# Optimization experiments

Hardware: AMD Instinct MI355X
Metric: run time of the kernel (lower is better)

Reference implementation:

```python
import jax, jax.numpy as jnp
import numpy as np

B, S, D = 2, 2048, 1024
M = 2048          # d_mlp
E = 8             # num_experts
TOP_K = 2


def setup_inputs() -> dict:
    key = jax.random.key(0)
    ks = jax.random.split(key, 5)
    std = 0.02
    return {
        "residual": jax.random.normal(ks[0], (B, S, D), jnp.float32),
        "W_router": jax.random.normal(ks[1], (D, E), jnp.float32) * std,
        "W_gate": jax.random.normal(ks[2], (E, D, M), jnp.float32) * std,
        "b_gate": jnp.zeros((E, M), jnp.float32),
        "W_up": jax.random.normal(ks[3], (E, D, M), jnp.float32) * std,
        "b_up": jnp.zeros((E, M), jnp.float32),
        "W_out": jax.random.normal(ks[4], (E, M, D), jnp.float32) * std,
        "b_out": jnp.zeros((E, D), jnp.float32),
    }


def reference(residual, W_router, W_gate, b_gate, W_up, b_up, W_out, b_out):
    # --- router: softmax over experts, top-k selection, renormalize ---
    router_logits = jnp.einsum('bsd,de->bse', residual, W_router)
    router_probs = jax.nn.softmax(router_logits, axis=-1)
    top_k_probs, top_k_idx = jax.lax.top_k(router_probs, TOP_K)          # [B,S,K]
    top_k_probs = top_k_probs / (jnp.sum(top_k_probs, -1, keepdims=True) + 1e-8)
    # per-expert combine weight [B,S,E]; top-k indices are unique per token
    one_hot = jax.nn.one_hot(top_k_idx, E, dtype=residual.dtype)          # [B,S,K,E]
    expert_weights = jnp.einsum('bsk,bske->bse', top_k_probs, one_hot)
    # --- each expert runs dense SwiGLU MLP on the FULL batch (compute-then-mask, as in source) ---
    gate = jax.nn.silu(jnp.einsum('bsd,edm->ebsm', residual, W_gate) + b_gate[:, None, None, :])
    up = jnp.einsum('bsd,edm->ebsm', residual, W_up) + b_up[:, None, None, :]
    hidden = gate * up                                                    # [E,B,S,M]
    expert_out = jnp.einsum('ebsm,emd->ebsd', hidden, W_out) + b_out[:, None, None, :]
    # --- weighted combine (weights are zero for non-selected experts) ---
    output = jnp.einsum('bse,ebsd->bsd', expert_weights, expert_out)
    return output
```

## Files before the change

kernel.cpp:

```cpp
#include <hip/hip_runtime.h>
#include <cstdint>
#include <cstddef>

#define TT 4096
#define DD 1024
#define MM 2048
#define EE 8
#define NPAIR 8192

typedef unsigned short u16;
typedef __bf16 bf16x8 __attribute__((ext_vector_type(8)));
typedef float f32x4 __attribute__((ext_vector_type(4)));
typedef __attribute__((address_space(3))) void* lds_vp;
typedef __attribute__((address_space(1))) const void* gbl_cvp;

__device__ __forceinline__ void async16(u16* l, const u16* g) {
  __builtin_amdgcn_global_load_lds((gbl_cvp)(const void*)g, (lds_vp)(void*)l, 16, 0, 0);
}

__device__ __forceinline__ u16 f2bf(float f) {
  uint32_t u = __builtin_bit_cast(uint32_t, f);
  u += 0x7fffu + ((u >> 16) & 1u);
  return (u16)(u >> 16);
}
__device__ __forceinline__ float bf2f(u16 h) {
  uint32_t u = ((uint32_t)h) << 16;
  return __builtin_bit_cast(float, u);
}

__global__ void router_kernel(const float* __restrict__ X, const float* __restrict__ Wr,
                              int* __restrict__ tok_idx, float* __restrict__ wpair) {
  int wave = threadIdx.x >> 6;
  int lane = threadIdx.x & 63;
  int t = blockIdx.x * 4 + wave;
  const float4* x4 = (const float4*)(X + (size_t)t * DD);
  float acc[EE];
#pragma unroll
  for (int e = 0; e < EE; e++) acc[e] = 0.f;
#pragma unroll
  for (int i = 0; i < 4; i++) {
    float4 xv = x4[i * 64 + lane];
    const float4* wr4 = (const float4*)(Wr + (size_t)(i * 256 + lane * 4) * EE);
    float xs[4] = {xv.x, xv.y, xv.z, xv.w};
#pragma unroll
    for (int c = 0; c < 4; c++) {
      float4 wa = wr4[c * 2 + 0];
      float4 wb = wr4[c * 2 + 1];
      acc[0] += xs[c] * wa.x; acc[1] += xs[c] * wa.y;
      acc[2] += xs[c] * wa.z; acc[3] += xs[c] * wa.w;
      acc[4] += xs[c] * wb.x; acc[5] += xs[c] * wb.y;
      acc[6] += xs[c] * wb.z; acc[7] += xs[c] * wb.w;
    }
  }
#pragma unroll
  for (int off = 32; off > 0; off >>= 1)
#pragma unroll
    for (int e = 0; e < EE; e++) acc[e] += __shfl_xor(acc[e], off);
  if (lane == 0) {
    float mx = acc[0];
#pragma unroll
    for (int e = 1; e < EE; e++) mx = fmaxf(mx, acc[e]);
    float p[EE], s = 0.f;
#pragma unroll
    for (int e = 0; e < EE; e++) { p[e] = __expf(acc[e] - mx); s += p[e]; }
    float inv = 1.f / s;
#pragma unroll
    for (int e = 0; e < EE; e++) p[e] *= inv;
    int i0 = 0;
#pragma unroll
    for (int e = 1; e < EE; e++) if (p[e] > p[i0]) i0 = e;
    int i1 = (i0 == 0) ? 1 : 0;
#pragma unroll
    for (int e = 0; e < EE; e++) if (e != i0 && p[e] > p[i1]) i1 = e;
    float denom = p[i0] + p[i1] + 1e-8f;
    tok_idx[t * 2 + 0] = i0;
    tok_idx[t * 2 + 1] = i1;
    wpair[t * 2 + 0] = p[i0] / denom;
    wpair[t * 2 + 1] = p[i1] / denom;
  }
}

__global__ void bucket_kernel(const int* __restrict__ tok_idx, int* __restrict__ offsets,
                              int* __restrict__ bucket) {
  __shared__ int lcnt[EE];
  __shared__ int lcur[EE];
  int tid = threadIdx.x;
  if (tid < EE) lcnt[tid] = 0;
  __syncthreads();
  for (int i = tid; i < NPAIR; i += 1024) atomicAdd(&lcnt[tok_idx[i]], 1);
  __syncthreads();
  if (tid == 0) {
    int s = 0;
    for (int e = 0; e < EE; e++) {
      offsets[e] = s;
      lcur[e] = s;
      s += lcnt[e];
    }
    offsets[EE] = s;
  }
  __syncthreads();
  for (int i = tid; i < NPAIR; i += 1024) {
    int e = tok_idx[i];
    int pos = atomicAdd(&lcur[e], 1);
    bucket[pos] = i;
  }
}

__global__ void cvtx_kernel(const float* __restrict__ X, u16* __restrict__ Xbf) {
  int i = blockIdx.x * 256 + threadIdx.x;
  float4 v = ((const float4*)X)[i];
  ushort4 o;
  o.x = f2bf(v.x); o.y = f2bf(v.y); o.z = f2bf(v.z); o.w = f2bf(v.w);
  ((ushort4*)Xbf)[i] = o;
}

__global__ void transpose_cvt(const float* __restrict__ in, u16* __restrict__ out, int R, int C) {
  __shared__ float tile[32][33];
  int e = blockIdx.z;
  const float* I = in + (size_t)e * R * C;
  u16* O = out + (size_t)e * R * C;
  int c0 = blockIdx.x * 32, r0 = blockIdx.y * 32;
  for (int i = threadIdx.y; i < 32; i += 8)
    tile[i][threadIdx.x] = I[(size_t)(r0 + i) * C + c0 + threadIdx.x];
  __syncthreads();
  for (int i = threadIdx.y; i < 32; i += 8)
    O[(size_t)(c0 + i) * R + r0 + threadIdx.x] = f2bf(tile[threadIdx.x][i]);
}

template <int MODE>
__global__ __launch_bounds__(256)
void moe_gemm(const u16* __restrict__ Aglob, const u16* __restrict__ Wt,
              const float* __restrict__ bias, u16* __restrict__ Hws,
              float* __restrict__ Ypart, const int* __restrict__ offsets,
              const int* __restrict__ bucket, const float* __restrict__ wpair) {
  constexpr int K = (MODE == 2) ? MM : DD;
  constexpr int N = (MODE == 2) ? DD : MM;

  int x = blockIdx.x;
  int expert = -1, row0 = 0, rows = 0;
#pragma unroll 1
  for (int e = 0; e < EE; e++) {
    int o0 = offsets[e], o1 = offsets[e + 1];
    int nt = (o1 - o0 + 127) >> 7;
    if (x < nt) { expert = e; row0 = o0 + (x << 7); rows = min(128, o1 - row0); break; }
    x -= nt;
  }
  if (expert < 0) return;
  int n0 = blockIdx.y * 128;

  __shared__ u16 Alds[128 * 32];
  __shared__ u16 Blds[128 * 32];

  int tid = threadIdx.x;
  int wave = tid >> 6, lane = tid & 63;
  int wm = wave >> 1, wn = wave & 1;
  int quad = lane >> 4, l15 = lane & 15;

  long arow0, arow1;
  {
    int r0l = wave * 32 + (lane >> 2);
    int r1l = r0l + 16;
    int rr0 = min(r0l, rows - 1);
    int rr1 = min(r1l, rows - 1);
    if (MODE == 2) {
      arow0 = (long)(row0 + rr0) * K;
      arow1 = (long)(row0 + rr1) * K;
    } else {
      arow0 = (long)(bucket[row0 + rr0] >> 1) * K;
      arow1 = (long)(bucket[row0 + rr1] >> 1) * K;
    }
  }
  const u16* Wbase = Wt + (size_t)expert * N * K + (size_t)n0 * K;
  int brow = wave * 32 + (lane >> 2);
  int lchunk = (lane & 3) * 8;

  f32x4 acc[4][4];
#pragma unroll
  for (int i = 0; i < 4; i++)
#pragma unroll
    for (int j = 0; j < 4; j++) acc[i][j] = (f32x4){0.f, 0.f, 0.f, 0.f};

  for (int k0 = 0; k0 < K; k0 += 32) {
    async16(&Alds[(wave * 32) * 32], Aglob + arow0 + k0 + lchunk);
    async16(&Alds[(wave * 32 + 16) * 32], Aglob + arow1 + k0 + lchunk);
    async16(&Blds[(wave * 32) * 32], Wbase + (long)brow * K + k0 + lchunk);
    async16(&Blds[(wave * 32 + 16) * 32], Wbase + (long)(brow + 16) * K + k0 + lchunk);
    __syncthreads();
    bf16x8 af[4], bfr[4];
#pragma unroll
    for (int i = 0; i < 4; i++) {
      af[i]  = *(const bf16x8*)&Alds[(wm * 64 + i * 16 + l15) * 32 + quad * 8];
      bfr[i] = *(const bf16x8*)&Blds[(wn * 64 + i * 16 + l15) * 32 + quad * 8];
    }
#pragma unroll
    for (int i = 0; i < 4; i++)
#pragma unroll
      for (int j = 0; j < 4; j++)
        acc[i][j] = __builtin_amdgcn_mfma_f32_16x16x32_bf16(af[i], bfr[j], acc[i][j], 0, 0, 0);
    __syncthreads();
  }

#pragma unroll
  for (int i = 0; i < 4; i++) {
    int lrb = wm * 64 + i * 16 + quad * 4;
#pragma unroll
    for (int j = 0; j < 4; j++) {
      int gc = n0 + wn * 64 + j * 16 + l15;
      float bv = bias[expert * N + gc];
#pragma unroll
      for (int r = 0; r < 4; r++) {
        int lr = lrb + r;
        if (lr < rows) {
          int grow = row0 + lr;
          float v = acc[i][j][r] + bv;
          if (MODE == 0) {
            Hws[(size_t)grow * MM + gc] = f2bf(v);
          } else if (MODE == 1) {
            float u = bf2f(Hws[(size_t)grow * MM + gc]);
            float sg = v / (1.f + __expf(-v));
            Hws[(size_t)grow * MM + gc] = f2bf(sg * u);
          } else {
            int p = bucket[grow];
            float w = wpair[p];
            Ypart[(size_t)p * DD + gc] = w * v;
          }
        }
      }
    }
  }
}

__global__ void combine_kernel(const float* __restrict__ Ypart, float* __restrict__ out) {
  int i = blockIdx.x * 256 + threadIdx.x;
  int t = i >> 8;
  int c4 = i & 255;
  const float4* y0 = (const float4*)(Ypart + (size_t)(2 * t) * DD) + c4;
  const float4* y1 = (const float4*)(Ypart + (size_t)(2 * t + 1) * DD) + c4;
  float4 a = *y0, b = *y1;
  float4 o;
  o.x = a.x + b.x; o.y = a.y + b.y; o.z = a.z + b.z; o.w = a.w + b.w;
  ((float4*)out)[i] = o;
}

extern "C" void kernel_launch(void* const* d_in, const int* in_sizes, int n_in,
                              void* d_out, int out_size, void* d_ws, size_t ws_size,
                              hipStream_t stream) {
  const float* residual = (const float*)d_in[0];
  const float* W_router = (const float*)d_in[1];
  const float* W_gate   = (const float*)d_in[2];
  const float* b_gate   = (const float*)d_in[3];
  const float* W_up     = (const float*)d_in[4];
  const float* b_up     = (const float*)d_in[5];
  const float* W_out    = (const float*)d_in[6];
  const float* b_out    = (const float*)d_in[7];
  float* out = (float*)d_out;

  char* ws = (char*)d_ws;
  int*   tok_idx = (int*)(ws + 0);
  float* wpair   = (float*)(ws + 32768);
  int*   offsets = (int*)(ws + 65536);
  int*   bucket  = (int*)(ws + 65536 + 512);
  u16*   Xbf  = (u16*)(ws + 131072);
  u16*   WtG  = Xbf + (size_t)TT * DD;
  u16*   WtU  = WtG + (size_t)EE * MM * DD;
  u16*   WtO  = WtU + (size_t)EE * MM * DD;
  u16*   Hws  = WtO + (size_t)EE * DD * MM;
  float* Ypart = (float*)(Hws + (size_t)NPAIR * MM);

  cvtx_kernel<<<dim3(TT * DD / 4 / 256), dim3(256), 0, stream>>>(residual, Xbf);
  transpose_cvt<<<dim3(MM / 32, DD / 32, EE), dim3(32, 8), 0, stream>>>(W_gate, WtG, DD, MM);
  transpose_cvt<<<dim3(MM / 32, DD / 32, EE), dim3(32, 8), 0, stream>>>(W_up,   WtU, DD, MM);
  transpose_cvt<<<dim3(DD / 32, MM / 32, EE), dim3(32, 8), 0, stream>>>(W_out,  WtO, MM, DD);
  router_kernel<<<dim3(TT / 4), dim3(256), 0, stream>>>(residual, W_router, tok_idx, wpair);
  bucket_kernel<<<dim3(1), dim3(1024), 0, stream>>>(tok_idx, offsets, bucket);
  moe_gemm<0><<<dim3(72, MM / 128), dim3(256), 0, stream>>>(Xbf, WtU, b_up,  Hws, Ypart, offsets, bucket, wpair);
  moe_gemm<1><<<dim3(72, MM / 128), dim3(256), 0, stream>>>(Xbf, WtG, b_gate, Hws, Ypart, offsets, bucket, wpair);
  moe_gemm<2><<<dim3(72, DD / 128), dim3(256), 0, stream>>>(Hws, WtO, b_out, Hws, Ypart, offsets, bucket, wpair);
  combine_kernel<<<dim3(TT * DD / 4 / 256), dim3(256), 0, stream>>>(Ypart, out);
}
```

Baseline: 529.0 us.

## Fuse gate/up GEMMs, swizzle LDS, and atomically combine expert outputs

Merges the separate up and gate GEMM passes into one kernel that shares the A tile and computes SiLU(g)*u in the epilogue. This removes the bf16 round-trip of the up result through Hws and one full pass over X. The output GEMM now atomically adds weighted results straight into the zeroed output, dropping the Ypart buffer and the combine kernel. An XOR swizzle on LDS chunk placement is added to cut bank conflicts. The costs are doubled accumulator registers in the fused kernel, which may lower occupancy, and fp32 atomic traffic in place of plain stores.

```diff
diff --git a/kernel.cpp b/kernel.cpp
--- a/kernel.cpp
+++ b/kernel.cpp
@@ -22,10 +22,6 @@
   uint32_t u = __builtin_bit_cast(uint32_t, f);
   u += 0x7fffu + ((u >> 16) & 1u);
   return (u16)(u >> 16);
-}
-__device__ __forceinline__ float bf2f(u16 h) {
-  uint32_t u = ((uint32_t)h) << 16;
-  return __builtin_bit_cast(float, u);
 }
 
 __global__ void router_kernel(const float* __restrict__ X, const float* __restrict__ Wr,
@@ -127,76 +123,87 @@
     O[(size_t)(c0 + i) * R + r0 + threadIdx.x] = f2bf(tile[threadIdx.x][i]);
 }
 
-template <int MODE>
-__global__ __launch_bounds__(256)
-void moe_gemm(const u16* __restrict__ Aglob, const u16* __restrict__ Wt,
-              const float* __restrict__ bias, u16* __restrict__ Hws,
-              float* __restrict__ Ypart, const int* __restrict__ offsets,
-              const int* __restrict__ bucket, const float* __restrict__ wpair) {
-  constexpr int K = (MODE == 2) ? MM : DD;
-  constexpr int N = (MODE == 2) ? DD : MM;
-
-  int x = blockIdx.x;
-  int expert = -1, row0 = 0, rows = 0;
+__device__ __forceinline__ bool tile_map(const int* __restrict__ offsets, int x,
+                                         int& expert, int& row0, int& rows) {
+  expert = -1;
 #pragma unroll 1
   for (int e = 0; e < EE; e++) {
     int o0 = offsets[e], o1 = offsets[e + 1];
     int nt = (o1 - o0 + 127) >> 7;
-    if (x < nt) { expert = e; row0 = o0 + (x << 7); rows = min(128, o1 - row0); break; }
+    if (x < nt) { expert = e; row0 = o0 + (x << 7); rows = min(128, o1 - row0); return true; }
     x -= nt;
   }
-  if (expert < 0) return;
+  return false;
+}
+
+
+__global__ __launch_bounds__(256)
+void moe_gemm_gu(const u16* __restrict__ Xbf, const u16* __restrict__ Wg,
+                 const float* __restrict__ bgate, const float* __restrict__ bup,
+                 u16* __restrict__ Hws, const int* __restrict__ offsets,
+                 const int* __restrict__ bucket) {
+  constexpr int K = DD, N = MM;
+  int expert, row0, rows;
+  if (!tile_map(offsets, blockIdx.x, expert, row0, rows)) return;
   int n0 = blockIdx.y * 128;
 
   __shared__ u16 Alds[128 * 32];
-  __shared__ u16 Blds[128 * 32];
+  __shared__ u16 Glds[128 * 32];
+  __shared__ u16 Ulds[128 * 32];
 
   int tid = threadIdx.x;
   int wave = tid >> 6, lane = tid & 63;
   int wm = wave >> 1, wn = wave & 1;
   int quad = lane >> 4, l15 = lane & 15;
+  int swz = ((lane & 3) ^ ((lane >> 3) & 3)) * 8;
+  int rp  = (quad ^ ((l15 >> 1) & 3)) * 8;
 
   long arow0, arow1;
   {
     int r0l = wave * 32 + (lane >> 2);
-    int r1l = r0l + 16;
     int rr0 = min(r0l, rows - 1);
-    int rr1 = min(r1l, rows - 1);
-    if (MODE == 2) {
-      arow0 = (long)(row0 + rr0) * K;
-      arow1 = (long)(row0 + rr1) * K;
-    } else {
-      arow0 = (long)(bucket[row0 + rr0] >> 1) * K;
-      arow1 = (long)(bucket[row0 + rr1] >> 1) * K;
-    }
-  }
-  const u16* Wbase = Wt + (size_t)expert * N * K + (size_t)n0 * K;
-  int brow = wave * 32 + (lane >> 2);
-  int lchunk = (lane & 3) * 8;
-
-  f32x4 acc[4][4];
+    int rr1 = min(r0l + 16, rows - 1);
+    arow0 = (long)(bucket[row0 + rr0] >> 1) * K;
+    arow1 = (long)(bucket[row0 + rr1] >> 1) * K;
+  }
+  const u16* A0 = Xbf + arow0 + swz;
+  const u16* A1 = Xbf + arow1 + swz;
+  long woff = (size_t)expert * N * K + (size_t)n0 * K + (long)(wave * 32 + (lane >> 2)) * K + swz;
+  const u16* G0 = Wg + woff;
+  const u16* G1 = G0 + 16 * K;
+  const u16* U0 = G0 + (size_t)EE * MM * DD;
+  const u16* U1 = U0 + 16 * K;
+
+  u16* sA0 = &Alds[(wave * 32) * 32];      u16* sA1 = &Alds[(wave * 32 + 16) * 32];
+  u16* sG0 = &Glds[(wave * 32) * 32];      u16* sG1 = &Glds[(wave * 32 + 16) * 32];
+  u16* sU0 = &Ulds[(wave * 32) * 32];      u16* sU1 = &Ulds[(wave * 32 + 16) * 32];
+
+  f32x4 ag[4][4], au[4][4];
 #pragma unroll
   for (int i = 0; i < 4; i++)
 #pragma unroll
-    for (int j = 0; j < 4; j++) acc[i][j] = (f32x4){0.f, 0.f, 0.f, 0.f};
+    for (int j = 0; j < 4; j++) { ag[i][j] = (f32x4){0,0,0,0}; au[i][j] = (f32x4){0,0,0,0}; }
 
   for (int k0 = 0; k0 < K; k0 += 32) {
-    async16(&Alds[(wave * 32) * 32], Aglob + arow0 + k0 + lchunk);
-    async16(&Alds[(wave * 32 + 16) * 32], Aglob + arow1 + k0 + lchunk);
-    async16(&Blds[(wave * 32) * 32], Wbase + (long)brow * K + k0 + lchunk);
-    async16(&Blds[(wave * 32 + 16) * 32], Wbase + (long)(brow + 16) * K + k0 + lchunk);
+    async16(sA0, A0); async16(sA1, A1);
+    async16(sG0, G0); async16(sG1, G1);
+    async16(sU0, U0); async16(sU1, U1);
+    A0 += 32; A1 += 32; G0 += 32; G1 += 32; U0 += 32; U1 += 32;
     __syncthreads();
-    bf16x8 af[4], bfr[4];
+    bf16x8 af[4], bg[4], bu[4];
 #pragma unroll
     for (int i = 0; i < 4; i++) {
-      af[i]  = *(const bf16x8*)&Alds[(wm * 64 + i * 16 + l15) * 32 + quad * 8];
-      bfr[i] = *(const bf16x8*)&Blds[(wn * 64 + i * 16 + l15) * 32 + quad * 8];
+      af[i] = *(const bf16x8*)&Alds[(wm * 64 + i * 16 + l15) * 32 + rp];
+      bg[i] = *(const bf16x8*)&Glds[(wn * 64 + i * 16 + l15) * 32 + rp];
+      bu[i] = *(const bf16x8*)&Ulds[(wn * 64 + i * 16 + l15) * 32 + rp];
     }
 #pragma unroll
     for (int i = 0; i < 4; i++)
 #pragma unroll
-      for (int j = 0; j < 4; j++)
-        acc[i][j] = __builtin_amdgcn_mfma_f32_16x16x32_bf16(af[i], bfr[j], acc[i][j], 0, 0, 0);
+      for (int j = 0; j < 4; j++) {
+        ag[i][j] = __builtin_amdgcn_mfma_f32_16x16x32_bf16(af[i], bg[j], ag[i][j], 0, 0, 0);
+        au[i][j] = __builtin_amdgcn_mfma_f32_16x16x32_bf16(af[i], bu[j], au[i][j], 0, 0, 0);
+      }
     __syncthreads();
   }
 
@@ -206,40 +213,103 @@
 #pragma unroll
     for (int j = 0; j < 4; j++) {
       int gc = n0 + wn * 64 + j * 16 + l15;
-      float bv = bias[expert * N + gc];
+      float bgv = bgate[expert * N + gc];
+      float buv = bup[expert * N + gc];
 #pragma unroll
       for (int r = 0; r < 4; r++) {
         int lr = lrb + r;
         if (lr < rows) {
           int grow = row0 + lr;
-          float v = acc[i][j][r] + bv;
-          if (MODE == 0) {
-            Hws[(size_t)grow * MM + gc] = f2bf(v);
-          } else if (MODE == 1) {
-            float u = bf2f(Hws[(size_t)grow * MM + gc]);
-            float sg = v / (1.f + __expf(-v));
-            Hws[(size_t)grow * MM + gc] = f2bf(sg * u);
-          } else {
-            int p = bucket[grow];
-            float w = wpair[p];
-            Ypart[(size_t)p * DD + gc] = w * v;
-          }
+          float g = ag[i][j][r] + bgv;
+          float u = au[i][j][r] + buv;
+          float h = (g / (1.f + __expf(-g))) * u;
+          Hws[(size_t)grow * MM + gc] = f2bf(h);
         }
       }
     }
   }
 }
 
-__global__ void combine_kernel(const float* __restrict__ Ypart, float* __restrict__ out) {
-  int i = blockIdx.x * 256 + threadIdx.x;
-  int t = i >> 8;
-  int c4 = i & 255;
-  const float4* y0 = (const float4*)(Ypart + (size_t)(2 * t) * DD) + c4;
-  const float4* y1 = (const float4*)(Ypart + (size_t)(2 * t + 1) * DD) + c4;
-  float4 a = *y0, b = *y1;
-  float4 o;
-  o.x = a.x + b.x; o.y = a.y + b.y; o.z = a.z + b.z; o.w = a.w + b.w;
-  ((float4*)out)[i] = o;
+__global__ __launch_bounds__(256)
+void moe_gemm_out(const u16* __restrict__ Hws, const u16* __restrict__ Wo,
+                  const float* __restrict__ bout, float* __restrict__ out,
+                  const int* __restrict__ offsets, const int* __restrict__ bucket,
+                  const float* __restrict__ wpair) {
+  constexpr int K = MM, N = DD;
+  int expert, row0, rows;
+  if (!tile_map(offsets, blockIdx.x, expert, row0, rows)) return;
+  int n0 = blockIdx.y * 128;
+
+  __shared__ u16 Alds[128 * 32];
+  __shared__ u16 Blds[128 * 32];
+
+  int tid = threadIdx.x;
+  int wave = tid >> 6, lane = tid & 63;
+  int wm = wave >> 1, wn = wave & 1;
+  int quad = lane >> 4, l15 = lane & 15;
+  int swz = ((lane & 3) ^ ((lane >> 3) & 3)) * 8;
+  int rp  = (quad ^ ((l15 >> 1) & 3)) * 8;
+
+  long arow0, arow1;
+  {
+    int r0l = wave * 32 + (lane >> 2);
+    int rr0 = min(r0l, rows - 1);
+    int rr1 = min(r0l + 16, rows - 1);
+    arow0 = (long)(row0 + rr0) * K;
+    arow1 = (long)(row0 + rr1) * K;
+  }
+  const u16* A0 = Hws + arow0 + swz;
+  const u16* A1 = Hws + arow1 + swz;
+  const u16* B0 = Wo + (size_t)expert * N * K + (size_t)n0 * K + (long)(wave * 32 + (lane >> 2)) * K + swz;
+  const u16* B1 = B0 + 16 * K;
+
+  u16* sA0 = &Alds[(wave * 32) * 32]; u16* sA1 = &Alds[(wave * 32 + 16) * 32];
+  u16* sB0 = &Blds[(wave * 32) * 32]; u16* sB1 = &Blds[(wave * 32 + 16) * 32];
+
+  f32x4 acc[4][4];
+#pragma unroll
+  for (int i = 0; i < 4; i++)
+#pragma unroll
+    for (int j = 0; j < 4; j++) acc[i][j] = (f32x4){0, 0, 0, 0};
+
+  for (int k0 = 0; k0 < K; k0 += 32) {
+    async16(sA0, A0); async16(sA1, A1);
+    async16(sB0, B0); async16(sB1, B1);
+    A0 += 32; A1 += 32; B0 += 32; B1 += 32;
+    __syncthreads();
+    bf16x8 af[4], bf[4];
+#pragma unroll
+    for (int i = 0; i < 4; i++) {
+      af[i] = *(const bf16x8*)&Alds[(wm * 64 + i * 16 + l15) * 32 + rp];
+      bf[i] = *(const bf16x8*)&Blds[(wn * 64 + i * 16 + l15) * 32 + rp];
+    }
+#pragma unroll
+    for (int i = 0; i < 4; i++)
+#pragma unroll
+      for (int j = 0; j < 4; j++)
+        acc[i][j] = __builtin_amdgcn_mfma_f32_16x16x32_bf16(af[i], bf[j], acc[i][j], 0, 0, 0);
+    __syncthreads();
+  }
+
+#pragma unroll
+  for (int i = 0; i < 4; i++) {
+    int lrb = wm * 64 + i * 16 + quad * 4;
+#pragma unroll
+    for (int j = 0; j < 4; j++) {
+      int gc = n0 + wn * 64 + j * 16 + l15;
+      float bv = bout[expert * N + gc];
+#pragma unroll
+      for (int r = 0; r < 4; r++) {
+        int lr = lrb + r;
+        if (lr < rows) {
+          int grow = row0 + lr;
+          int p = bucket[grow];
+          float w = wpair[p];
+          atomicAdd(&out[(size_t)(p >> 1) * DD + gc], w * (acc[i][j][r] + bv));
+        }
+      }
+    }
+  }
 }
 
 extern "C" void kernel_launch(void* const* d_in, const int* in_sizes, int n_in,
@@ -265,7 +335,8 @@
   u16*   WtU  = WtG + (size_t)EE * MM * DD;
   u16*   WtO  = WtU + (size_t)EE * MM * DD;
   u16*   Hws  = WtO + (size_t)EE * DD * MM;
-  float* Ypart = (float*)(Hws + (size_t)NPAIR * MM);
+
+  hipMemsetAsync(out, 0, (size_t)out_size * sizeof(float), stream);
 
   cvtx_kernel<<<dim3(TT * DD / 4 / 256), dim3(256), 0, stream>>>(residual, Xbf);
   transpose_cvt<<<dim3(MM / 32, DD / 32, EE), dim3(32, 8), 0, stream>>>(W_gate, WtG, DD, MM);
@@ -273,8 +344,6 @@
   transpose_cvt<<<dim3(DD / 32, MM / 32, EE), dim3(32, 8), 0, stream>>>(W_out,  WtO, MM, DD);
   router_kernel<<<dim3(TT / 4), dim3(256), 0, stream>>>(residual, W_router, tok_idx, wpair);
   bucket_kernel<<<dim3(1), dim3(1024), 0, stream>>>(tok_idx, offsets, bucket);
-  moe_gemm<0><<<dim3(72, MM / 128), dim3(256), 0, stream>>>(Xbf, WtU, b_up,  Hws, Ypart, offsets, bucket, wpair);
-  moe_gemm<1><<<dim3(72, MM / 128), dim3(256), 0, stream>>>(Xbf, WtG, b_gate, Hws, Ypart, offsets, bucket, wpair);
-  moe_gemm<2><<<dim3(72, DD / 128), dim3(256), 0, stream>>>(Hws, WtO, b_out, Hws, Ypart, offsets, bucket, wpair);
-  combine_kernel<<<dim3(TT * DD / 4 / 256), dim3(256), 0, stream>>>(Ypart, out);
-}
+  moe_gemm_gu<<<dim3(72, MM / 128), dim3(256), 0, stream>>>(Xbf, WtG, b_gate, b_up, Hws, offsets, bucket);
+  moe_gemm_out<<<dim3(72, DD / 128), dim3(256), 0, stream>>>(Hws, WtO, b_out, out, offsets, bucket, wpair);
+}
```

After: 610.3 us. 15.4% more time.
